# Optimization experiments

Measured on AMD Instinct MI355X. Metric: run time of the kernel, lower is better.

The kernel has to match this reference:

```python
import jax, jax.numpy as jnp
import numpy as np

N = 100000
IN_C, HID_C, OUT_C = 256, 128, 2
E = 3200000


def setup_inputs() -> dict:
    key = jax.random.key(0)
    ks = jax.random.split(key, 8)
    x = jax.random.normal(ks[0], (N, IN_C), dtype=jnp.float32)
    edge_index = jax.random.randint(ks[1], (2, E), 0, N, dtype=jnp.int64)
    edge_weight = jax.random.uniform(ks[2], (E,), dtype=jnp.float32)
    # GCNConv params (Glorot-ish init)
    W1 = jax.random.normal(ks[3], (IN_C, HID_C), dtype=jnp.float32) / np.sqrt(IN_C)
    b1 = jnp.zeros((HID_C,), dtype=jnp.float32)
    W2 = jax.random.normal(ks[4], (HID_C, OUT_C), dtype=jnp.float32) / np.sqrt(HID_C)
    b2 = jnp.zeros((OUT_C,), dtype=jnp.float32)
    return {"x": x, "edge_index": edge_index, "edge_weight": edge_weight,
            "W1": W1, "b1": b1, "W2": W2, "b2": b2}


def _gcn_norm(edge_index, edge_weight, num_nodes):
    # Add self-loops with weight 1 (PyG GCNConv default), then symmetric norm.
    loop = jnp.arange(num_nodes, dtype=edge_index.dtype)
    src = jnp.concatenate([edge_index[0], loop])
    dst = jnp.concatenate([edge_index[1], loop])
    w = jnp.concatenate([edge_weight, jnp.ones((num_nodes,), edge_weight.dtype)])
    deg = jax.ops.segment_sum(w, dst, num_segments=num_nodes)
    dinv = jnp.where(deg > 0, jax.lax.rsqrt(deg), 0.0)
    norm = dinv[src] * w * dinv[dst]
    return src, dst, norm


def _gcn_conv(x, src, dst, norm, W, b):
    h = x @ W                                   # [N, C_out] dense transform first
    msg = norm[:, None] * h[src]                # [E+N, C_out] gather + scale
    agg = jax.ops.segment_sum(msg, dst, num_segments=x.shape[0])
    return agg + b


def reference(x, edge_index, edge_weight, W1, b1, W2, b2):
    src, dst, norm = _gcn_norm(edge_index, edge_weight, x.shape[0])
    h = jax.nn.relu(_gcn_conv(x, src, dst, norm, W1, b1))
    # dropout p=0.5 is identity in eval mode
    out = _gcn_conv(h, src, dst, norm, W2, b2)
    return out
```

## Files before the change

### kernel.cpp

```cpp
#include <hip/hip_runtime.h>
#include <hip/hip_fp16.h>

#define IN_C  256
#define HID_C 128
#define OUT_C 2
#define BSH   7
#define NB    128
#define BCAP  6144

typedef __attribute__((ext_vector_type(8))) short short8;
typedef __attribute__((ext_vector_type(4))) float float4v;

__device__ __forceinline__ unsigned short f2bf(float f) {
    unsigned u = __float_as_uint(f);
    unsigned r = 0x7fffu + ((u >> 16) & 1u);
    return (unsigned short)((u + r) >> 16);
}
__device__ __forceinline__ unsigned pk2(float a, float b) {
    return (unsigned)f2bf(a) | ((unsigned)f2bf(b) << 16);
}
__device__ __forceinline__ unsigned enc_edge(int src, float w) {
    unsigned h = (unsigned)(__half_as_ushort(__float2half(w)) & 0x7FFF);
    return (h << 17) | (unsigned)src;
}
__device__ __forceinline__ void dec_edge(unsigned rec, int& s, float& w) {
    s = (int)(rec & 0x1FFFFu);
    __half hh;
    *(unsigned short*)&hh = (unsigned short)(rec >> 17);
    w = __half2float(hh);
}

__global__ void k_wT(const float* __restrict__ W1, unsigned short* __restrict__ w1t) {
    int i = blockIdx.x * 256 + threadIdx.x;
    if (i >= HID_C * IN_C) return;
    int c = i >> 8, k = i & 255;
    w1t[i] = f2bf(W1[(size_t)k * HID_C + c]);
}

__global__ __launch_bounds__(256) void k_count(const int* __restrict__ ei,
                                               int* __restrict__ gcnt,
                                               int E, int K, int W, int CHv) {
    extern __shared__ int lh[];
    int w = blockIdx.x, t = threadIdx.x;
    for (int b = t; b < K; b += 256) lh[b] = 0;
    __syncthreads();
    int j0 = w * CHv;
    int j1 = min(j0 + CHv, E);
    for (int j = j0 + t; j < j1; j += 256)
        atomicAdd(&lh[ei[E + j] >> BSH], 1);
    __syncthreads();
    for (int b = t; b < K; b += 256) gcnt[(size_t)b * W + w] = lh[b];
}

__global__ __launch_bounds__(256) void k_scanA4(const int* __restrict__ cnt,
                                                int* __restrict__ excl,
                                                int* __restrict__ bsum, int n) {
    __shared__ int ss[256];
    int t = threadIdx.x;
    int base = blockIdx.x * 4096 + t * 16;
    int v[16]; int s = 0;
#pragma unroll
    for (int q = 0; q < 16; q++) { v[q] = (base + q < n) ? cnt[base + q] : 0; s += v[q]; }
    ss[t] = s;
    __syncthreads();
    for (int d = 1; d < 256; d <<= 1) {
        int x = (t >= d) ? ss[t - d] : 0;
        __syncthreads();
        ss[t] += x;
        __syncthreads();
    }
    int pre = (t == 0) ? 0 : ss[t - 1];
    if (t == 255) bsum[blockIdx.x] = ss[255];
    int run = pre;
#pragma unroll
    for (int q = 0; q < 16; q++) { if (base + q < n) excl[base + q] = run; run += v[q]; }
}

__global__ __launch_bounds__(256) void k_scanB(int* __restrict__ bsum, int nb) {
    __shared__ int ss[256];
    int t = threadIdx.x;
    int v = (t < nb) ? bsum[t] : 0;
    ss[t] = v;
    __syncthreads();
    for (int d = 1; d < 256; d <<= 1) {
        int x = (t >= d) ? ss[t - d] : 0;
        __syncthreads();
        ss[t] += x;
        __syncthreads();
    }
    if (t < nb) bsum[t] = ss[t] - v;
}

__global__ void k_scanC4(int* __restrict__ gpos, const int* __restrict__ bsum, int n) {
    int i = blockIdx.x * 256 + threadIdx.x;
    if (i < n) gpos[i] += bsum[i >> 12];
}

__global__ __launch_bounds__(256) void k_place(const int* __restrict__ ei,
                                               const float* __restrict__ w,
                                               const int* __restrict__ gpos,
                                               int2* __restrict__ ebuf,
                                               int E, int K, int W, int CHv) {
    extern __shared__ int lc[];
    int wg = blockIdx.x, t = threadIdx.x;
    for (int b = t; b < K; b += 256) lc[b] = gpos[(size_t)b * W + wg];
    __syncthreads();
    int j0 = wg * CHv;
    int j1 = min(j0 + CHv, E);
    for (int j = j0 + t; j < j1; j += 256) {
        int s = ei[j], d = ei[E + j];
        float wv = w[j];
        int pos = atomicAdd(&lc[d >> BSH], 1);
        ebuf[pos] = make_int2(s | ((d & (NB - 1)) << 17), __float_as_int(wv));
    }
}

__global__ __launch_bounds__(256) void k_bucket(const int2* __restrict__ ebuf,
                                                const int* __restrict__ gpos,
                                                unsigned* __restrict__ epack,
                                                int* __restrict__ rowptr,
                                                float* __restrict__ dinv,
                                                int W, int K, int E, int N) {
    __shared__ int2 ls[BCAP];
    __shared__ int lh[NB], lex[NB], lc[NB];
    int b = blockIdx.x, t = threadIdx.x;
    int base = gpos[(size_t)b * W];
    int next = (b + 1 < K) ? gpos[(size_t)(b + 1) * W] : E;
    int cnt = next - base;
    for (int i = t; i < NB; i += 256) lh[i] = 0;
    __syncthreads();
    if (cnt <= BCAP) {
        for (int j = t; j < cnt; j += 256)
            atomicAdd(&lh[(ebuf[base + j].x >> 17) & (NB - 1)], 1);
        __syncthreads();
        if (t == 0) {
            int run = 0;
            for (int i = 0; i < NB; i++) { lex[i] = run; lc[i] = run; run += lh[i]; }
        }
        __syncthreads();
        for (int j = t; j < cnt; j += 256) {
            int2 e = ebuf[base + j];
            int pos = atomicAdd(&lc[(e.x >> 17) & (NB - 1)], 1);
            ls[pos] = make_int2(e.x & 0x1FFFF, e.y);
        }
        __syncthreads();
        for (int j = t; j < cnt; j += 256) {
            int2 e = ls[j];
            epack[base + j] = enc_edge(e.x, __int_as_float(e.y));
        }
        for (int r = t; r < NB; r += 256) {
            int node = b * NB + r;
            if (node < N) {
                rowptr[node] = base + lex[r];
                float s = 1.0f;
                int rb = lex[r], re = rb + lh[r];
                for (int j = rb; j < re; j++) s += __int_as_float(ls[j].y);
                dinv[node] = s > 0.f ? rsqrtf(s) : 0.f;
            }
        }
    } else {
        for (int j = base + t; j < next; j += 256)
            atomicAdd(&lh[(ebuf[j].x >> 17) & (NB - 1)], 1);
        __syncthreads();
        if (t == 0) {
            int run = 0;
            for (int i = 0; i < NB; i++) { lex[i] = run; lc[i] = run; run += lh[i]; }
        }
        __syncthreads();
        for (int j = base + t; j < next; j += 256) {
            int2 e = ebuf[j];
            int pos = base + atomicAdd(&lc[(e.x >> 17) & (NB - 1)], 1);
            epack[pos] = enc_edge(e.x & 0x1FFFF, __int_as_float(e.y));
        }
        __syncthreads();
        for (int r = t; r < NB; r += 256) {
            int node = b * NB + r;
            if (node < N) {
                int rb = base + lex[r], re = rb + lh[r];
                rowptr[node] = rb;
                float s = 1.0f;
                for (int j = rb; j < re; j++) {
                    int ss; float wv;
                    dec_edge(epack[j], ss, wv);
                    s += wv;
                }
                dinv[node] = s > 0.f ? rsqrtf(s) : 0.f;
            }
        }
    }
    if (b == K - 1 && t == 0) rowptr[N] = E;
}

__global__ void k_scale(unsigned* __restrict__ epack, const float* __restrict__ dinv, int E) {
    int i = blockIdx.x * 256 + threadIdx.x;
    if (i >= E) return;
    unsigned rec = epack[i];
    int src; float wv;
    dec_edge(rec, src, wv);
    epack[i] = enc_edge(src, wv * dinv[src]);
}

#define XS_LD 36
#define WT_LD 260
__global__ __launch_bounds__(256) void k_gemm1(const float* __restrict__ x,
                                               const unsigned short* __restrict__ w1t,
                                               unsigned short* __restrict__ h1b, int n) {
    __shared__ __align__(16) unsigned short wt[HID_C * WT_LD];
    __shared__ __align__(16) unsigned short xs[64 * XS_LD];
    int tid  = threadIdx.x;
    int row0 = blockIdx.x * 64;
    for (int it = 0; it < 16; it++) {
        int idx = it * 256 + tid;
        int c = idx >> 5, kc = idx & 31;
        uint4 v = *(const uint4*)(w1t + (size_t)c * IN_C + kc * 8);
        uint2* dst = (uint2*)(wt + c * WT_LD + kc * 8);
        dst[0] = make_uint2(v.x, v.y);
        dst[1] = make_uint2(v.z, v.w);
    }
    int wv = tid >> 6, ln = tid & 63;
    int m = ln & 15, quad = ln >> 4;
    float4v acc[8];
#pragma unroll
    for (int ct = 0; ct < 8; ct++) acc[ct] = (float4v){0.f, 0.f, 0.f, 0.f};

    for (int k0 = 0; k0 < IN_C; k0 += 32) {
        __syncthreads();
        {
            int r = tid >> 2, s4 = tid & 3;
            int gr = row0 + r; if (gr >= n) gr = n - 1;
            const float4* px = (const float4*)(x + (size_t)gr * IN_C + k0 + s4 * 8);
            float4 a = px[0], bq = px[1];
            uint2* d = (uint2*)(xs + r * XS_LD + s4 * 8);
            d[0] = make_uint2(pk2(a.x, a.y), pk2(a.z, a.w));
            d[1] = make_uint2(pk2(bq.x, bq.y), pk2(bq.z, bq.w));
        }
        __syncthreads();
        union { uint2 u[2]; short8 v; } af;
        const uint2* pa = (const uint2*)(xs + (wv * 16 + m) * XS_LD + quad * 8);
        af.u[0] = pa[0]; af.u[1] = pa[1];
#pragma unroll
        for (int ct = 0; ct < 8; ct++) {
            union { uint2 u[2]; short8 v; } bf;
            const uint2* pb = (const uint2*)(wt + (ct * 16 + m) * WT_LD + k0 + quad * 8);
            bf.u[0] = pb[0]; bf.u[1] = pb[1];
            acc[ct] = __builtin_amdgcn_mfma_f32_16x16x32_bf16(af.v, bf.v, acc[ct], 0, 0, 0);
        }
    }
    __syncthreads();
    unsigned short* ot = wt;
#pragma unroll
    for (int ct = 0; ct < 8; ct++)
#pragma unroll
        for (int r = 0; r < 4; r++)
            ot[(wv * 16 + quad * 4 + r) * 136 + ct * 16 + m] = f2bf(acc[ct][r]);
    __syncthreads();
#pragma unroll
    for (int p = 0; p < 4; p++) {
        int idx = p * 256 + tid;
        int r = idx >> 4, c8 = idx & 15;
        if (row0 + r < n)
            *(uint4*)(h1b + (size_t)(row0 + r) * HID_C + c8 * 8) =
                *(const uint4*)(ot + r * 136 + c8 * 8);
    }
}

__global__ __launch_bounds__(256) void k_agg1(const int* __restrict__ rowptr,
                                              const unsigned* __restrict__ epack,
                                              const unsigned short* __restrict__ h1b,
                                              const float* __restrict__ dinv,
                                              const float* __restrict__ b1,
                                              const float* __restrict__ W2,
                                              float* __restrict__ h2, int n) {
    int wid  = (blockIdx.x * 256 + threadIdx.x) >> 6;
    int lane = threadIdx.x & 63;
    if (wid >= n) return;
    int beg = rowptr[wid], end = rowptr[wid + 1];
    float ax = 0.f, ay = 0.f;
    int j = beg;
    for (; j + 16 <= end; j += 16) {
        int   es[16]; float ew[16];
        unsigned p[16];
#pragma unroll
        for (int q = 0; q < 16; q++) dec_edge(epack[j + q], es[q], ew[q]);
#pragma unroll
        for (int q = 0; q < 16; q++)
            p[q] = *((const unsigned*)(h1b + (size_t)es[q] * HID_C) + lane);
#pragma unroll
        for (int q = 0; q < 16; q++) {
            ax = fmaf(ew[q], __uint_as_float(p[q] << 16), ax);
            ay = fmaf(ew[q], __uint_as_float(p[q] & 0xffff0000u), ay);
        }
    }
    for (; j + 4 <= end; j += 4) {
        int   es[4]; float ew[4];
        unsigned p[4];
#pragma unroll
        for (int q = 0; q < 4; q++) dec_edge(epack[j + q], es[q], ew[q]);
#pragma unroll
        for (int q = 0; q < 4; q++)
            p[q] = *((const unsigned*)(h1b + (size_t)es[q] * HID_C) + lane);
#pragma unroll
        for (int q = 0; q < 4; q++) {
            ax = fmaf(ew[q], __uint_as_float(p[q] << 16), ax);
            ay = fmaf(ew[q], __uint_as_float(p[q] & 0xffff0000u), ay);
        }
    }
    for (; j < end; j++) {
        int es; float ewv;
        dec_edge(epack[j], es, ewv);
        unsigned p0 = *((const unsigned*)(h1b + (size_t)es * HID_C) + lane);
        ax = fmaf(ewv, __uint_as_float(p0 << 16), ax);
        ay = fmaf(ewv, __uint_as_float(p0 & 0xffff0000u), ay);
    }
    float di = dinv[wid]; float sc = di * di;
    unsigned ps = *((const unsigned*)(h1b + (size_t)wid * HID_C) + lane);
    float2 bv = ((const float2*)b1)[lane];
    float ox = bv.x + sc * __uint_as_float(ps << 16)         + di * ax;
    float oy = bv.y + sc * __uint_as_float(ps & 0xffff0000u) + di * ay;
    ox = fmaxf(ox, 0.f);
    oy = fmaxf(oy, 0.f);
    float4 w4 = *((const float4*)(W2 + 4 * lane));
    float s0 = ox * w4.x + oy * w4.z;
    float s1 = ox * w4.y + oy * w4.w;
#pragma unroll
    for (int d = 32; d > 0; d >>= 1) {
        s0 += __shfl_xor(s0, d);
        s1 += __shfl_xor(s1, d);
    }
    if (lane == 0)
        ((float2*)h2)[wid] = make_float2(s0, s1);
}

__global__ __launch_bounds__(256) void k_agg2(const int* __restrict__ rowptr,
                                              const unsigned* __restrict__ epack,
                                              const float* __restrict__ h2,
                                              const float* __restrict__ dinv,
                                              const float* __restrict__ b2,
                                              float* __restrict__ out, int n) {
    int wid  = (blockIdx.x * 256 + threadIdx.x) >> 6;
    int lane = threadIdx.x & 63;
    if (wid >= n) return;
    int beg = rowptr[wid], end = rowptr[wid + 1];
    float sx = 0.f, sy = 0.f;
    for (int j = beg + lane; j < end; j += 64) {
        int es; float nm;
        dec_edge(epack[j], es, nm);
        float2 v = ((const float2*)h2)[es];
        sx = fmaf(nm, v.x, sx);
        sy = fmaf(nm, v.y, sy);
    }
#pragma unroll
    for (int d = 32; d > 0; d >>= 1) {
        sx += __shfl_xor(sx, d);
        sy += __shfl_xor(sy, d);
    }
    if (lane == 0) {
        float di = dinv[wid]; float sc = di * di;
        float2 hv = ((const float2*)h2)[wid];
        ((float2*)out)[wid] = make_float2(b2[0] + sc * hv.x + di * sx,
                                          b2[1] + sc * hv.y + di * sy);
    }
}

extern "C" void kernel_launch(void* const* d_in, const int* in_sizes, int n_in,
                              void* d_out, int out_size, void* d_ws, size_t ws_size,
                              hipStream_t stream) {
    const float* x  = (const float*)d_in[0];
    const int*   ei = (const int*)d_in[1];
    const float* ew = (const float*)d_in[2];
    const float* W1 = (const float*)d_in[3];
    const float* b1 = (const float*)d_in[4];
    const float* W2 = (const float*)d_in[5];
    const float* b2 = (const float*)d_in[6];
    float* out = (float*)d_out;

    int N = in_sizes[0] / IN_C;
    int E = in_sizes[2];
    int K = (N + NB - 1) >> BSH;
    int W = 256;
    int CHv = (E + W - 1) / W;
    int KW = K * W;

    char* ws = (char*)d_ws;
    float* dinv   = (float*)ws; ws += (size_t)N * 4;
    int*   rowptr = (int*)ws;   ws += (size_t)(N + 1) * 4 + 4;
    int*   gcnt   = (int*)ws;   ws += (size_t)KW * 4;
    int*   bsum   = (int*)ws;   ws += 1024;
    int2*  ebuf   = (int2*)ws;  ws += (size_t)E * 8;
    unsigned* epack = (unsigned*)ws; ws += (size_t)E * 4;
    unsigned short* w1t = (unsigned short*)ws; ws += (size_t)HID_C * IN_C * 2;
    unsigned short* h1b = (unsigned short*)ws; ws += (size_t)N * HID_C * 2;
    float* h2     = (float*)ws; ws += (size_t)N * OUT_C * 4;

    int nb_e  = (E + 255) / 256;
    int nb_s4 = (KW + 4095) / 4096;
    int nb_sc = (KW + 255) / 256;
    int nb_w  = (N * 64 + 255) / 256;
    size_t lds_k = (size_t)K * 4;

    k_wT    <<<(HID_C * IN_C + 255) / 256, 256, 0, stream>>>(W1, w1t);
    k_count <<<W, 256, lds_k, stream>>>(ei, gcnt, E, K, W, CHv);
    k_scanA4<<<nb_s4, 256, 0, stream>>>(gcnt, gcnt, bsum, KW);
    k_scanB <<<1, 256, 0, stream>>>(bsum, nb_s4);
    k_scanC4<<<nb_sc, 256, 0, stream>>>(gcnt, bsum, KW);
    k_place <<<W, 256, lds_k, stream>>>(ei, ew, gcnt, ebuf, E, K, W, CHv);
    k_bucket<<<K, 256, 0, stream>>>(ebuf, gcnt, epack, rowptr, dinv, W, K, E, N);
    k_scale <<<nb_e, 256, 0, stream>>>(epack, dinv, E);
    k_gemm1 <<<(N + 63) / 64, 256, 0, stream>>>(x, w1t, h1b, N);
    k_agg1  <<<nb_w, 256, 0, stream>>>(rowptr, epack, h1b, dinv, b1, W2, h2, N);
    k_agg2  <<<nb_w, 256, 0, stream>>>(rowptr, epack, h2, dinv, b2, out, N);
}
```

Before: 503.1 us.

## Fold source dinv into GEMM output, drop edge-scale pass, widen agg1 gathers

```diff
diff --git a/kernel.cpp b/kernel.cpp
--- a/kernel.cpp
+++ b/kernel.cpp
@@ -28,6 +28,17 @@
     __half hh;
     *(unsigned short*)&hh = (unsigned short)(rec >> 17);
     w = __half2float(hh);
+}
+__device__ __forceinline__ void up8(uint4 p, float* f) {
+    f[0] = __uint_as_float(p.x << 16); f[1] = __uint_as_float(p.x & 0xffff0000u);
+    f[2] = __uint_as_float(p.y << 16); f[3] = __uint_as_float(p.y & 0xffff0000u);
+    f[4] = __uint_as_float(p.z << 16); f[5] = __uint_as_float(p.z & 0xffff0000u);
+    f[6] = __uint_as_float(p.w << 16); f[7] = __uint_as_float(p.w & 0xffff0000u);
+}
+__device__ __forceinline__ void fma8(float* ac, uint4 p, float w) {
+    float t[8]; up8(p, t);
+#pragma unroll
+    for (int k = 0; k < 8; k++) ac[k] = fmaf(w, t[k], ac[k]);
 }
 
 __global__ void k_wT(const float* __restrict__ W1, unsigned short* __restrict__ w1t) {
@@ -191,19 +202,11 @@
     if (b == K - 1 && t == 0) rowptr[N] = E;
 }
 
-__global__ void k_scale(unsigned* __restrict__ epack, const float* __restrict__ dinv, int E) {
-    int i = blockIdx.x * 256 + threadIdx.x;
-    if (i >= E) return;
-    unsigned rec = epack[i];
-    int src; float wv;
-    dec_edge(rec, src, wv);
-    epack[i] = enc_edge(src, wv * dinv[src]);
-}
-
 #define XS_LD 36
 #define WT_LD 260
 __global__ __launch_bounds__(256) void k_gemm1(const float* __restrict__ x,
                                                const unsigned short* __restrict__ w1t,
+                                               const float* __restrict__ dinv,
                                                unsigned short* __restrict__ h1b, int n) {
     __shared__ __align__(16) unsigned short wt[HID_C * WT_LD];
     __shared__ __align__(16) unsigned short xs[64 * XS_LD];
@@ -247,12 +250,14 @@
         }
     }
     __syncthreads();
+    float4 dv = *(const float4*)(dinv + row0 + wv * 16 + quad * 4);
+    const float* dvf = (const float*)&dv;
     unsigned short* ot = wt;
 #pragma unroll
     for (int ct = 0; ct < 8; ct++)
 #pragma unroll
         for (int r = 0; r < 4; r++)
-            ot[(wv * 16 + quad * 4 + r) * 136 + ct * 16 + m] = f2bf(acc[ct][r]);
+            ot[(wv * 16 + quad * 4 + r) * 136 + ct * 16 + m] = f2bf(acc[ct][r] * dvf[r]);
     __syncthreads();
 #pragma unroll
     for (int p = 0; p < 4; p++) {
@@ -274,61 +279,64 @@
     int wid  = (blockIdx.x * 256 + threadIdx.x) >> 6;
     int lane = threadIdx.x & 63;
     if (wid >= n) return;
+    int q   = lane >> 4;
+    int c16 = lane & 15;
     int beg = rowptr[wid], end = rowptr[wid + 1];
-    float ax = 0.f, ay = 0.f;
+    float ac[8];
+#pragma unroll
+    for (int k = 0; k < 8; k++) ac[k] = 0.f;
     int j = beg;
-    for (; j + 16 <= end; j += 16) {
-        int   es[16]; float ew[16];
-        unsigned p[16];
-#pragma unroll
-        for (int q = 0; q < 16; q++) dec_edge(epack[j + q], es[q], ew[q]);
-#pragma unroll
-        for (int q = 0; q < 16; q++)
-            p[q] = *((const unsigned*)(h1b + (size_t)es[q] * HID_C) + lane);
-#pragma unroll
-        for (int q = 0; q < 16; q++) {
-            ax = fmaf(ew[q], __uint_as_float(p[q] << 16), ax);
-            ay = fmaf(ew[q], __uint_as_float(p[q] & 0xffff0000u), ay);
-        }
-    }
-    for (; j + 4 <= end; j += 4) {
-        int   es[4]; float ew[4];
-        unsigned p[4];
-#pragma unroll
-        for (int q = 0; q < 4; q++) dec_edge(epack[j + q], es[q], ew[q]);
-#pragma unroll
-        for (int q = 0; q < 4; q++)
-            p[q] = *((const unsigned*)(h1b + (size_t)es[q] * HID_C) + lane);
-#pragma unroll
-        for (int q = 0; q < 4; q++) {
-            ax = fmaf(ew[q], __uint_as_float(p[q] << 16), ax);
-            ay = fmaf(ew[q], __uint_as_float(p[q] & 0xffff0000u), ay);
-        }
-    }
-    for (; j < end; j++) {
-        int es; float ewv;
-        dec_edge(epack[j], es, ewv);
-        unsigned p0 = *((const unsigned*)(h1b + (size_t)es * HID_C) + lane);
-        ax = fmaf(ewv, __uint_as_float(p0 << 16), ax);
-        ay = fmaf(ewv, __uint_as_float(p0 & 0xffff0000u), ay);
-    }
-    float di = dinv[wid]; float sc = di * di;
-    unsigned ps = *((const unsigned*)(h1b + (size_t)wid * HID_C) + lane);
-    float2 bv = ((const float2*)b1)[lane];
-    float ox = bv.x + sc * __uint_as_float(ps << 16)         + di * ax;
-    float oy = bv.y + sc * __uint_as_float(ps & 0xffff0000u) + di * ay;
-    ox = fmaxf(ox, 0.f);
-    oy = fmaxf(oy, 0.f);
-    float4 w4 = *((const float4*)(W2 + 4 * lane));
-    float s0 = ox * w4.x + oy * w4.z;
-    float s1 = ox * w4.y + oy * w4.w;
-#pragma unroll
-    for (int d = 32; d > 0; d >>= 1) {
+    for (; j + 8 <= end; j += 8) {
+        unsigned r0 = epack[j + q];
+        unsigned r1 = epack[j + 4 + q];
+        int s0, s1; float w0, w1;
+        dec_edge(r0, s0, w0);
+        dec_edge(r1, s1, w1);
+        uint4 p0 = *(const uint4*)(h1b + (size_t)s0 * HID_C + c16 * 8);
+        uint4 p1 = *(const uint4*)(h1b + (size_t)s1 * HID_C + c16 * 8);
+        fma8(ac, p0, w0);
+        fma8(ac, p1, w1);
+    }
+    for (; j < end; j += 4) {
+        int jj = j + q;
+        if (jj < end) {
+            unsigned r0 = epack[jj];
+            int s0; float w0;
+            dec_edge(r0, s0, w0);
+            uint4 p0 = *(const uint4*)(h1b + (size_t)s0 * HID_C + c16 * 8);
+            fma8(ac, p0, w0);
+        }
+    }
+#pragma unroll
+    for (int k = 0; k < 8; k++) {
+        ac[k] += __shfl_xor(ac[k], 16);
+        ac[k] += __shfl_xor(ac[k], 32);
+    }
+    float di = dinv[wid];
+    uint4 ps = *(const uint4*)(h1b + (size_t)wid * HID_C + c16 * 8);
+    float sf[8]; up8(ps, sf);
+    float4 ba = *(const float4*)(b1 + c16 * 8);
+    float4 bb = *(const float4*)(b1 + c16 * 8 + 4);
+    const float* bap = (const float*)&ba;
+    const float* bbp = (const float*)&bb;
+    float o[8];
+#pragma unroll
+    for (int k = 0; k < 4; k++) o[k]     = fmaxf(fmaf(di, ac[k] + sf[k], bap[k]), 0.f);
+#pragma unroll
+    for (int k = 0; k < 4; k++) o[k + 4] = fmaxf(fmaf(di, ac[k + 4] + sf[k + 4], bbp[k]), 0.f);
+    const float4* wp = (const float4*)(W2 + 16 * c16);
+    float4 wa = wp[0], wb = wp[1], wc = wp[2], wd = wp[3];
+    float s0 = o[0] * wa.x + o[1] * wa.z + o[2] * wb.x + o[3] * wb.z
+             + o[4] * wc.x + o[5] * wc.z + o[6] * wd.x + o[7] * wd.z;
+    float s1 = o[0] * wa.y + o[1] * wa.w + o[2] * wb.y + o[3] * wb.w
+             + o[4] * wc.y + o[5] * wc.w + o[6] * wd.y + o[7] * wd.w;
+#pragma unroll
+    for (int d = 8; d > 0; d >>= 1) {
         s0 += __shfl_xor(s0, d);
         s1 += __shfl_xor(s1, d);
     }
     if (lane == 0)
-        ((float2*)h2)[wid] = make_float2(s0, s1);
+        ((float2*)h2)[wid] = make_float2(di * s0, di * s1);
 }
 
 __global__ __launch_bounds__(256) void k_agg2(const int* __restrict__ rowptr,
@@ -355,10 +363,10 @@
         sy += __shfl_xor(sy, d);
     }
     if (lane == 0) {
-        float di = dinv[wid]; float sc = di * di;
+        float di = dinv[wid];
         float2 hv = ((const float2*)h2)[wid];
-        ((float2*)out)[wid] = make_float2(b2[0] + sc * hv.x + di * sx,
-                                          b2[1] + sc * hv.y + di * sy);
+        ((float2*)out)[wid] = make_float2(b2[0] + di * (sx + hv.x),
+                                          b2[1] + di * (sy + hv.y));
     }
 }
 
@@ -383,7 +391,7 @@
 
     char* ws = (char*)d_ws;
     float* dinv   = (float*)ws; ws += (size_t)N * 4;
-    int*   rowptr = (int*)ws;   ws += (size_t)(N + 1) * 4 + 4;
+    int*   rowptr = (int*)ws;   ws += (size_t)(N + 1) * 4 + 4 + 8;
     int*   gcnt   = (int*)ws;   ws += (size_t)KW * 4;
     int*   bsum   = (int*)ws;   ws += 1024;
     int2*  ebuf   = (int2*)ws;  ws += (size_t)E * 8;
@@ -392,7 +400,6 @@
     unsigned short* h1b = (unsigned short*)ws; ws += (size_t)N * HID_C * 2;
     float* h2     = (float*)ws; ws += (size_t)N * OUT_C * 4;
 
-    int nb_e  = (E + 255) / 256;
     int nb_s4 = (KW + 4095) / 4096;
     int nb_sc = (KW + 255) / 256;
     int nb_w  = (N * 64 + 255) / 256;
@@ -405,8 +412,7 @@
     k_scanC4<<<nb_sc, 256, 0, stream>>>(gcnt, bsum, KW);
     k_place <<<W, 256, lds_k, stream>>>(ei, ew, gcnt, ebuf, E, K, W, CHv);
     k_bucket<<<K, 256, 0, stream>>>(ebuf, gcnt, epack, rowptr, dinv, W, K, E, N);
-    k_scale <<<nb_e, 256, 0, stream>>>(epack, dinv, E);
-    k_gemm1 <<<(N + 63) / 64, 256, 0, stream>>>(x, w1t, h1b, N);
+    k_gemm1 <<<(N + 63) / 64, 256, 0, stream>>>(x, w1t, dinv, h1b, N);
     k_agg1  <<<nb_w, 256, 0, stream>>>(rowptr, epack, h1b, dinv, b1, W2, h2, N);
     k_agg2  <<<nb_w, 256, 0, stream>>>(rowptr, epack, h2, dinv, b2, out, N);
 }
```

Measured after the change: 490.3 us. -2.5%, faster.
